# Optimization experiments

Hardware: AMD Instinct MI355X
Metric: run time of the kernel (lower is better)

The kernel has to match this reference:

```python
import jax, jax.numpy as jnp
import numpy as np

V, NJ, NCOMP, NBETA = 778, 16, 24, 10
F_CLOSED, N_ANCHOR = 1554, 32
B, NOBJ = 8, 16384
# MANO kinematic tree parents (wrist + 5 fingers x 3 joints)
PARENTS = np.array([-1, 0, 1, 2, 0, 4, 5, 0, 7, 8, 0, 10, 11, 0, 13, 14])


def setup_inputs() -> dict:
    key = jax.random.key(0)
    ks = jax.random.split(key, 12)
    hand_pose = jax.random.normal(ks[0], (B, 3 + 3 + NCOMP), jnp.float32) * 0.1
    obj_points = jax.random.normal(ks[1], (B, NOBJ, 3), jnp.float32) * 0.1
    hand_beta = jax.random.normal(ks[2], (B, NBETA), jnp.float32) * 0.5
    v_template = jax.random.normal(ks[3], (V, 3), jnp.float32) * 0.05
    shapedirs = jax.random.normal(ks[4], (V, 3, NBETA), jnp.float32) * 0.01
    posedirs = jax.random.normal(ks[5], (V, 3, (NJ - 1) * 9), jnp.float32) * 0.01
    J_regressor = jax.nn.softmax(jax.random.normal(ks[6], (NJ, V), jnp.float32), axis=-1)
    lbs_weights = jax.nn.softmax(jax.random.normal(ks[7], (V, NJ), jnp.float32) * 2.0, axis=-1)
    pca_comps = jax.random.normal(ks[8], (NCOMP, (NJ - 1) * 3), jnp.float32) * 0.1
    anchor_weights = jax.nn.softmax(jax.random.normal(ks[9], (N_ANCHOR, 3), jnp.float32), axis=-1)
    closed_faces = jax.random.randint(ks[10], (F_CLOSED, 3), 0, V, jnp.int32)
    anchor_face_idx = jax.random.randint(ks[11], (N_ANCHOR, 3), 0, V, jnp.int32)
    return dict(hand_pose=hand_pose, obj_points=obj_points, hand_beta=hand_beta,
                v_template=v_template, shapedirs=shapedirs, posedirs=posedirs,
                J_regressor=J_regressor, lbs_weights=lbs_weights, pca_comps=pca_comps,
                anchor_weights=anchor_weights, closed_faces=closed_faces,
                anchor_face_idx=anchor_face_idx)


def rodrigues(r):
    # r: [..., 3] axis-angle -> [..., 3, 3] rotation matrix
    theta = jnp.sqrt(jnp.sum(r * r, axis=-1, keepdims=True) + 1e-16)
    k = r / theta
    c = jnp.cos(theta)[..., None]
    s = jnp.sin(theta)[..., None]
    kx, ky, kz = k[..., 0], k[..., 1], k[..., 2]
    zero = jnp.zeros_like(kx)
    K = jnp.stack([zero, -kz, ky, kz, zero, -kx, -ky, kx, zero], axis=-1)
    K = K.reshape(r.shape[:-1] + (3, 3))
    I = jnp.eye(3, dtype=r.dtype)
    return c * I + s * K + (1.0 - c) * k[..., :, None] * k[..., None, :]


def mano_verts(hand_pose, hand_beta, v_template, shapedirs, posedirs,
               J_regressor, lbs_weights, pca_comps):
    b = hand_pose.shape[0]
    trans = hand_pose[:, :3]
    root = hand_pose[:, 3:6]
    hand45 = hand_pose[:, 6:] @ pca_comps  # PCA -> 45-dim pose (flat_hand_mean: no mean add)
    full = jnp.concatenate([root, hand45], axis=-1).reshape(b, NJ, 3)
    R = rodrigues(full)  # [B,16,3,3]
    v_shaped = v_template + jnp.einsum('vdk,bk->bvd', shapedirs, hand_beta)
    J = jnp.einsum('jv,bvd->bjd', J_regressor, v_shaped)  # [B,16,3]
    pose_feat = (R[:, 1:] - jnp.eye(3, dtype=R.dtype)).reshape(b, (NJ - 1) * 9)
    v_posed = v_shaped + jnp.einsum('vdp,bp->bvd', posedirs, pose_feat)

    def make44(Rj, tj):  # [B,3,3],[B,3] -> [B,4,4]
        T = jnp.zeros((b, 4, 4), R.dtype)
        return T.at[:, :3, :3].set(Rj).at[:, :3, 3].set(tj).at[:, 3, 3].set(1.0)

    Ts = [make44(R[:, 0], J[:, 0])]
    for j in range(1, NJ):  # fixed small kinematic chain
        p = int(PARENTS[j])
        Ts.append(jnp.einsum('bmn,bnk->bmk', Ts[p], make44(R[:, j], J[:, j] - J[:, p])))
    T = jnp.stack(Ts, axis=1)  # [B,16,4,4] global joint transforms
    corr = jnp.einsum('bjmn,bjn->bjm', T[..., :3, :3], J)
    A = T.at[..., :3, 3].add(-corr)  # relative-to-rest transforms
    Tw = jnp.einsum('vj,bjmn->bvmn', lbs_weights, A)  # per-vertex skinning transform
    verts = jnp.einsum('bvmn,bvn->bvm', Tw[..., :3, :3], v_posed) + Tw[..., :3, 3]
    return verts + trans[:, None, :]


def vertex_normals(verts, faces):  # verts [B,V,3], faces [F,3]
    def one(v):
        p0, p1, p2 = v[faces[:, 0]], v[faces[:, 1]], v[faces[:, 2]]
        fn = jnp.cross(p1 - p0, p2 - p0)
        vn = (jnp.zeros_like(v).at[faces[:, 0]].add(fn)
              .at[faces[:, 1]].add(fn).at[faces[:, 2]].add(fn))
        return vn / (jnp.linalg.norm(vn, axis=-1, keepdims=True) + 1e-8)
    return jax.vmap(one)(verts)


def reference(hand_pose, obj_points, hand_beta, v_template, shapedirs, posedirs,
              J_regressor, lbs_weights, pca_comps, anchor_weights,
              closed_faces, anchor_face_idx):
    verts = mano_verts(hand_pose, hand_beta, v_template, shapedirs, posedirs,
                       J_regressor, lbs_weights, pca_comps)  # [B,778,3]
    # get_NN: squared cdist obj->hand + argmin (the memory-bound bottleneck)
    d2 = (jnp.sum(obj_points * obj_points, -1, keepdims=True)
          + jnp.sum(verts * verts, -1)[:, None, :]
          - 2.0 * jnp.einsum('bnd,bvd->bnv', obj_points, verts))  # [B,NOBJ,778]
    nn_idx = jnp.argmin(d2, axis=-1)  # [B,NOBJ]
    nn_dist = jnp.take_along_axis(d2, nn_idx[..., None], axis=-1)[..., 0]
    # contact_map_of_m_to_n
    cmap = 1.0 - 2.0 * (jax.nn.sigmoid(100.0 * nn_dist) - 0.5)
    # inter_penetr_loss: interior obj points (behind nearest hand vertex normal)
    normals = vertex_normals(verts, closed_faces)
    nn_vert = jnp.take_along_axis(verts, nn_idx[..., None], axis=1)
    nn_norm = jnp.take_along_axis(normals, nn_idx[..., None], axis=1)
    interior = jnp.sum((nn_vert - obj_points) * nn_norm, axis=-1) > 0.0
    penetration = jnp.sum(jnp.where(interior, nn_dist, 0.0)) / hand_pose.shape[0]
    # AnchorLayer: barycentric anchor points on the hand surface
    contact_candidates = jnp.einsum('ak,bakd->bad', anchor_weights, verts[:, anchor_face_idx])
    return cmap, penetration, verts, contact_candidates
```

## Files before the change

kernel.cpp:

```cpp
#include <hip/hip_runtime.h>
#include <math.h>

#define NV 778
#define NJ 16
#define NCOMP 24
#define NBETA 10
#define FC 1554
#define NA 32
#define NB 8
#define NOBJ 16384
#define VD (NV*3)
#define BCH 584
#define NVQ 832
#define NG 104
#define NCB 132

__global__ __launch_bounds__(256) void k_blend(
    const float* __restrict__ hp, const float* __restrict__ pca,
    const float* __restrict__ vt, const float* __restrict__ sd,
    const float* __restrict__ pd, const float* __restrict__ beta,
    const float* __restrict__ Jreg,
    float* __restrict__ VP, float* __restrict__ C0, float* __restrict__ C1,
    float* __restrict__ pen)
{
    int bid = blockIdx.x;
    int t = threadIdx.x;
    int wid = t >> 6, lane = t & 63;

    if (bid >= NB*BCH) {
        int o = (bid - NB*BCH)*4 + wid;
        if (o < 528) {
            int jd, k;
            if (o < 48) { jd = o; k = -1; }
            else        { jd = (o-48)/NBETA; k = (o-48)%NBETA; }
            int j = jd/3, d = jd%3;
            const float* jr = Jreg + j*NV;
            float acc = 0.0f;
            for (int v = lane; v < NV; v += 64) {
                float x = (k < 0) ? vt[v*3+d] : sd[(v*3+d)*NBETA + k];
                acc += jr[v] * x;
            }
            #pragma unroll
            for (int off = 32; off; off >>= 1) acc += __shfl_down(acc, off, 64);
            if (lane == 0) { if (k < 0) C0[jd] = acc; else C1[jd*NBETA + k] = acc; }
        }
        return;
    }

    int b = bid / BCH, c = bid % BCH;
    __shared__ float h45[45];
    __shared__ float sR[NJ*9];
    __shared__ float spf[135];

    if (t < 45) {
        float acc = 0.0f;
        #pragma unroll
        for (int k = 0; k < NCOMP; ++k) acc += hp[b*30 + 6 + k] * pca[k*45 + t];
        h45[t] = acc;
    }
    __syncthreads();
    if (t < NJ) {
        float rx, ry, rz;
        if (t == 0) { rx = hp[b*30+3]; ry = hp[b*30+4]; rz = hp[b*30+5]; }
        else        { rx = h45[(t-1)*3]; ry = h45[(t-1)*3+1]; rz = h45[(t-1)*3+2]; }
        float th = sqrtf(rx*rx + ry*ry + rz*rz + 1e-16f);
        float kx = rx/th, ky = ry/th, kz = rz/th;
        float cc = cosf(th), s = sinf(th), o = 1.0f - cc;
        float R[9];
        R[0] = cc + o*kx*kx;     R[1] = -s*kz + o*kx*ky;  R[2] =  s*ky + o*kx*kz;
        R[3] =  s*kz + o*ky*kx;  R[4] = cc + o*ky*ky;     R[5] = -s*kx + o*ky*kz;
        R[6] = -s*ky + o*kz*kx;  R[7] =  s*kx + o*kz*ky;  R[8] = cc + o*kz*kz;
        #pragma unroll
        for (int i = 0; i < 9; ++i) sR[t*9+i] = R[i];
    }
    __syncthreads();
    if (t < 135) {
        int mn = t % 9;
        float d = (mn == 0 || mn == 4 || mn == 8) ? 1.0f : 0.0f;
        spf[t] = sR[9 + t] - d;
    }
    if (bid == 0 && t == 0) *pen = 0.0f;
    __syncthreads();

    int r = c*4 + wid;
    if (r < VD) {
        const float* p  = pd + r * 135;
        float accP = p[lane] * spf[lane] + p[lane+64] * spf[lane+64];
        accP += (lane < 7) ? p[lane+128] * spf[lane+128] : 0.0f;

        float accS = (lane < NBETA) ? sd[r*NBETA + lane] * beta[b*NBETA + lane] : 0.0f;

        #pragma unroll
        for (int off = 32; off; off >>= 1) {
            accP += __shfl_down(accP, off, 64);
            accS += __shfl_down(accS, off, 64);
        }
        if (lane == 0) VP[b*VD + r] = vt[r] + accS + accP;
    }
}

#define PROC1(vk, vidx) {                                                        \
    float d0 = fmaf(-ox0, (vk).x, (vk).w);                                       \
    d0 = fmaf(-oy0, (vk).y, d0); d0 = fmaf(-oz0, (vk).z, d0);                    \
    if (d0 < s0) { s0 = d0; j0 = (vidx); }                                       \
    float d1 = fmaf(-ox1, (vk).x, (vk).w);                                       \
    d1 = fmaf(-oy1, (vk).y, d1); d1 = fmaf(-oz1, (vk).z, d1);                    \
    if (d1 < s1) { s1 = d1; j1 = (vidx); } }

#define PROC8(buf, gbase) {                                                      \
    PROC1((buf)[0], (gbase)+0); PROC1((buf)[1], (gbase)+1);                      \
    PROC1((buf)[2], (gbase)+2); PROC1((buf)[3], (gbase)+3);                      \
    PROC1((buf)[4], (gbase)+4); PROC1((buf)[5], (gbase)+5);                      \
    PROC1((buf)[6], (gbase)+6); PROC1((buf)[7], (gbase)+7); }

__global__ __launch_bounds__(256) void k_mega2(
    const float* __restrict__ hp, const float* __restrict__ pca,
    const float* __restrict__ beta,
    const float* __restrict__ C0, const float* __restrict__ C1,
    const float* __restrict__ W, const float* __restrict__ VP,
    const int* __restrict__ faces, const float* __restrict__ aw,
    const int* __restrict__ afi, const float* __restrict__ obj,
    float* __restrict__ verts, float* __restrict__ cmap,
    float* __restrict__ contact, float* __restrict__ pen)
{
    int blk = blockIdx.x;
    int b = blk >> 5;
    int g = blk & 31;
    int t = threadIdx.x, lane = t & 63, wid = t >> 6;

    __shared__ float4 sPK[NVQ];
    __shared__ float sv[VD];
    __shared__ float sn[VD];
    __shared__ float sR[NJ*9];
    __shared__ float sJ[NJ*3];
    __shared__ float4 sA4[NJ*3];
    __shared__ float h45[45];
    __shared__ float wsum[4];

    int n0 = g*512 + t;
    int n1 = n0 + 256;
    const float* o0p = obj + (b*NOBJ + n0)*3;
    const float* o1p = obj + (b*NOBJ + n1)*3;
    float ox0 = o0p[0], oy0 = o0p[1], oz0 = o0p[2];
    float ox1 = o1p[0], oy1 = o1p[1], oz1 = o1p[2];

    if (t < 45) {
        float acc = 0.0f;
        #pragma unroll
        for (int k = 0; k < NCOMP; ++k) acc += hp[b*30 + 6 + k] * pca[k*45 + t];
        h45[t] = acc;
    }
    for (int i = t; i < VD; i += 256) sn[i] = 0.0f;
    if (t < NVQ - NV) sPK[NV + t] = make_float4(0.f, 0.f, 0.f, 1e30f);
    __syncthreads();

    if (t < NJ) {
        float rx, ry, rz;
        if (t == 0) { rx = hp[b*30+3]; ry = hp[b*30+4]; rz = hp[b*30+5]; }
        else        { rx = h45[(t-1)*3]; ry = h45[(t-1)*3+1]; rz = h45[(t-1)*3+2]; }
        float th = sqrtf(rx*rx + ry*ry + rz*rz + 1e-16f);
        float kx = rx/th, ky = ry/th, kz = rz/th;
        float cc = cosf(th), s = sinf(th), o = 1.0f - cc;
        sR[t*9+0] = cc + o*kx*kx;     sR[t*9+1] = -s*kz + o*kx*ky;  sR[t*9+2] =  s*ky + o*kx*kz;
        sR[t*9+3] =  s*kz + o*ky*kx;  sR[t*9+4] = cc + o*ky*ky;     sR[t*9+5] = -s*kx + o*ky*kz;
        sR[t*9+6] = -s*ky + o*kz*kx;  sR[t*9+7] =  s*kx + o*kz*ky;  sR[t*9+8] = cc + o*kz*kz;
    }
    if (t >= 64 && t < 64 + NJ*3) {
        int o = t - 64;
        float acc = C0[o];
        #pragma unroll
        for (int k = 0; k < NBETA; ++k) acc += C1[o*NBETA + k] * beta[b*NBETA + k];
        sJ[o] = acc;
    }
    __syncthreads();

    if (t < 3) {
        const int par[NJ] = {-1,0,1,2,0,4,5,0,7,8,0,10,11,0,13,14};
        int m = t;
        float Tr[NJ][3], Tt[NJ];
        Tr[0][0] = sR[m*3+0]; Tr[0][1] = sR[m*3+1]; Tr[0][2] = sR[m*3+2];
        Tt[0] = sJ[m];
        #pragma unroll
        for (int j = 1; j < NJ; ++j) {
            int p = par[j];
            float t0 = sJ[j*3+0] - sJ[p*3+0];
            float t1 = sJ[j*3+1] - sJ[p*3+1];
            float t2 = sJ[j*3+2] - sJ[p*3+2];
            float a0 = Tr[p][0], a1 = Tr[p][1], a2 = Tr[p][2];
            #pragma unroll
            for (int n = 0; n < 3; ++n)
                Tr[j][n] = a0*sR[j*9+n] + a1*sR[j*9+3+n] + a2*sR[j*9+6+n];
            Tt[j] = a0*t0 + a1*t1 + a2*t2 + Tt[p];
        }
        #pragma unroll
        for (int j = 0; j < NJ; ++j) {
            float corr = Tr[j][0]*sJ[j*3] + Tr[j][1]*sJ[j*3+1] + Tr[j][2]*sJ[j*3+2];
            sA4[j*3 + m] = make_float4(Tr[j][0], Tr[j][1], Tr[j][2], Tt[j] - corr);
        }
    }
    __syncthreads();

    float tx = hp[b*30+0], ty = hp[b*30+1], tz = hp[b*30+2];
    for (int v = t; v < NV; v += 256) {
        float4 r0 = make_float4(0,0,0,0), r1 = make_float4(0,0,0,0), r2 = make_float4(0,0,0,0);
        const float4* w4 = (const float4*)(W + v * NJ);
        #pragma unroll
        for (int q = 0; q < 4; ++q) {
            float4 wv = w4[q];
            #pragma unroll
            for (int jj = 0; jj < 4; ++jj) {
                int j = q*4 + jj;
                float wj = (jj==0)?wv.x:(jj==1)?wv.y:(jj==2)?wv.z:wv.w;
                float4 A0 = sA4[j*3+0], A1 = sA4[j*3+1], A2 = sA4[j*3+2];
                r0.x += wj*A0.x; r0.y += wj*A0.y; r0.z += wj*A0.z; r0.w += wj*A0.w;
                r1.x += wj*A1.x; r1.y += wj*A1.y; r1.z += wj*A1.z; r1.w += wj*A1.w;
                r2.x += wj*A2.x; r2.y += wj*A2.y; r2.z += wj*A2.z; r2.w += wj*A2.w;
            }
        }
        float px = VP[b*VD + v*3], py = VP[b*VD + v*3+1], pz = VP[b*VD + v*3+2];
        float x = r0.x*px + r0.y*py + r0.z*pz + r0.w + tx;
        float y = r1.x*px + r1.y*py + r1.z*pz + r1.w + ty;
        float z = r2.x*px + r2.y*py + r2.z*pz + r2.w + tz;
        sv[v*3] = x; sv[v*3+1] = y; sv[v*3+2] = z;
        sPK[v] = make_float4(x, y, z, 0.5f*(x*x + y*y + z*z));
        if (g == 0) {
            int i = b*NV + v;
            verts[i*3] = x; verts[i*3+1] = y; verts[i*3+2] = z;
        }
    }
    __syncthreads();

    for (int f = t; f < FC; f += 256) {
        int i0 = faces[f*3], i1 = faces[f*3+1], i2 = faces[f*3+2];
        float ax = sv[i1*3+0]-sv[i0*3+0], ay = sv[i1*3+1]-sv[i0*3+1], az = sv[i1*3+2]-sv[i0*3+2];
        float bx = sv[i2*3+0]-sv[i0*3+0], by = sv[i2*3+1]-sv[i0*3+1], bz = sv[i2*3+2]-sv[i0*3+2];
        float cx = ay*bz - az*by, cy = az*bx - ax*bz, cz = ax*by - ay*bx;
        atomicAdd(&sn[i0*3+0], cx); atomicAdd(&sn[i0*3+1], cy); atomicAdd(&sn[i0*3+2], cz);
        atomicAdd(&sn[i1*3+0], cx); atomicAdd(&sn[i1*3+1], cy); atomicAdd(&sn[i1*3+2], cz);
        atomicAdd(&sn[i2*3+0], cx); atomicAdd(&sn[i2*3+1], cy); atomicAdd(&sn[i2*3+2], cz);
    }
    __syncthreads();

    if (g == 0 && t < NA*3) {
        int a = t / 3, d = t % 3;
        float acc = 0.0f;
        #pragma unroll
        for (int k = 0; k < 3; ++k)
            acc += aw[a*3 + k] * sv[afi[a*3 + k]*3 + d];
        contact[b*NA*3 + t] = acc;
    }

    float s0 = 1e30f, s1 = 1e30f;
    int j0 = 0, j1 = 0;
    {
        float4 A[8], B[8];
        #pragma unroll
        for (int k = 0; k < 8; ++k) A[k] = sPK[k];
        for (int gg = 0; gg + 2 <= NG; gg += 2) {
            #pragma unroll
            for (int k = 0; k < 8; ++k) B[k] = sPK[(gg+1)*8 + k];
            PROC8(A, gg*8);
            if (gg + 2 < NG) {
                #pragma unroll
                for (int k = 0; k < 8; ++k) A[k] = sPK[(gg+2)*8 + k];
            }
            PROC8(B, (gg+1)*8);
        }
    }

    float osq0 = ox0*ox0 + oy0*oy0 + oz0*oz0;
    float d20 = 2.0f * s0 + osq0;
    cmap[b*NOBJ + n0] = 2.0f / (1.0f + __expf(100.0f * d20));
    float4 q0 = sPK[j0];
    float dp0 = (q0.x - ox0)*sn[j0*3+0] + (q0.y - oy0)*sn[j0*3+1] + (q0.z - oz0)*sn[j0*3+2];
    float p = (dp0 > 0.0f) ? d20 : 0.0f;

    float osq1 = ox1*ox1 + oy1*oy1 + oz1*oz1;
    float d21 = 2.0f * s1 + osq1;
    cmap[b*NOBJ + n1] = 2.0f / (1.0f + __expf(100.0f * d21));
    float4 q1 = sPK[j1];
    float dp1 = (q1.x - ox1)*sn[j1*3+0] + (q1.y - oy1)*sn[j1*3+1] + (q1.z - oz1)*sn[j1*3+2];
    p += (dp1 > 0.0f) ? d21 : 0.0f;

    for (int off = 32; off; off >>= 1) p += __shfl_down(p, off, 64);
    if (lane == 0) wsum[wid] = p;
    __syncthreads();
    if (t == 0) atomicAdd(pen, (wsum[0] + wsum[1] + wsum[2] + wsum[3]) * (1.0f / NB));
}

extern "C" void kernel_launch(void* const* d_in, const int* in_sizes, int n_in,
                              void* d_out, int out_size, void* d_ws, size_t ws_size,
                              hipStream_t stream)
{
    const float* hp    = (const float*)d_in[0];
    const float* obj   = (const float*)d_in[1];
    const float* beta  = (const float*)d_in[2];
    const float* vt    = (const float*)d_in[3];
    const float* sd    = (const float*)d_in[4];
    const float* pd    = (const float*)d_in[5];
    const float* Jreg  = (const float*)d_in[6];
    const float* W     = (const float*)d_in[7];
    const float* pca   = (const float*)d_in[8];
    const float* aw    = (const float*)d_in[9];
    const int*   faces = (const int*)d_in[10];
    const int*   afi   = (const int*)d_in[11];

    float* out     = (float*)d_out;
    float* cmap    = out;
    float* pen     = out + NB*NOBJ;
    float* verts   = out + NB*NOBJ + 1;
    float* contact = out + NB*NOBJ + 1 + NB*NV*3;

    float* ws   = (float*)d_ws;
    float* VP   = ws;
    float* C0   = VP + NB*VD;
    float* C1   = C0 + 48;

    k_blend<<<NB*BCH + NCB, 256, 0, stream>>>(hp, pca, vt, sd, pd, beta, Jreg,
                                              VP, C0, C1, pen);
    k_mega2<<<NB*32, 256, 0, stream>>>(hp, pca, beta, C0, C1, W, VP, faces, aw,
                                       afi, obj, verts, cmap, contact, pen);
}
```

Measured before the change: 141.7 us.

## Split mega kernel into skinning, face-normal, and NN kernels to remove redundant work

Before this change, each of the 32 blocks per batch recomputed skinning, vertex positions and face normals for all 778 vertices. The work is now split into three kernels. The first does skinning with each block handling one slice of vertices and writing packed vertices to the workspace. The second accumulates face normals into global memory with atomics and computes the anchor points. The third loads the packed vertices and normals into shared memory and runs the nearest-neighbour search. This removes the 32x redundant per-block preamble, at the cost of two extra launches and a round trip through global memory and global atomics.

```diff
diff --git a/kernel.cpp b/kernel.cpp
--- a/kernel.cpp
+++ b/kernel.cpp
@@ -14,6 +14,9 @@
 #define NVQ 832
 #define NG 104
 #define NCB 132
+#define VSL 25
+#define FSL 49
+#define ZSL 73
 
 __global__ __launch_bounds__(256) void k_blend(
     const float* __restrict__ hp, const float* __restrict__ pca,
@@ -99,59 +102,33 @@
     }
 }
 
-#define PROC1(vk, vidx) {                                                        \
-    float d0 = fmaf(-ox0, (vk).x, (vk).w);                                       \
-    d0 = fmaf(-oy0, (vk).y, d0); d0 = fmaf(-oz0, (vk).z, d0);                    \
-    if (d0 < s0) { s0 = d0; j0 = (vidx); }                                       \
-    float d1 = fmaf(-ox1, (vk).x, (vk).w);                                       \
-    d1 = fmaf(-oy1, (vk).y, d1); d1 = fmaf(-oz1, (vk).z, d1);                    \
-    if (d1 < s1) { s1 = d1; j1 = (vidx); } }
-
-#define PROC8(buf, gbase) {                                                      \
-    PROC1((buf)[0], (gbase)+0); PROC1((buf)[1], (gbase)+1);                      \
-    PROC1((buf)[2], (gbase)+2); PROC1((buf)[3], (gbase)+3);                      \
-    PROC1((buf)[4], (gbase)+4); PROC1((buf)[5], (gbase)+5);                      \
-    PROC1((buf)[6], (gbase)+6); PROC1((buf)[7], (gbase)+7); }
-
-__global__ __launch_bounds__(256) void k_mega2(
+__global__ __launch_bounds__(256) void k_skelp(
     const float* __restrict__ hp, const float* __restrict__ pca,
     const float* __restrict__ beta,
     const float* __restrict__ C0, const float* __restrict__ C1,
     const float* __restrict__ W, const float* __restrict__ VP,
-    const int* __restrict__ faces, const float* __restrict__ aw,
-    const int* __restrict__ afi, const float* __restrict__ obj,
-    float* __restrict__ verts, float* __restrict__ cmap,
-    float* __restrict__ contact, float* __restrict__ pen)
-{
-    int blk = blockIdx.x;
-    int b = blk >> 5;
-    int g = blk & 31;
-    int t = threadIdx.x, lane = t & 63, wid = t >> 6;
-
-    __shared__ float4 sPK[NVQ];
-    __shared__ float sv[VD];
-    __shared__ float sn[VD];
+    float* __restrict__ verts, float4* __restrict__ PK, float* __restrict__ NRM)
+{
+    int k = blockIdx.x;
+    int b = k >> 5, s = k & 31;
+    int t = threadIdx.x;
+    __shared__ float h45[45];
     __shared__ float sR[NJ*9];
     __shared__ float sJ[NJ*3];
     __shared__ float4 sA4[NJ*3];
-    __shared__ float h45[45];
-    __shared__ float wsum[4];
-
-    int n0 = g*512 + t;
-    int n1 = n0 + 256;
-    const float* o0p = obj + (b*NOBJ + n0)*3;
-    const float* o1p = obj + (b*NOBJ + n1)*3;
-    float ox0 = o0p[0], oy0 = o0p[1], oz0 = o0p[2];
-    float ox1 = o1p[0], oy1 = o1p[1], oz1 = o1p[2];
 
     if (t < 45) {
         float acc = 0.0f;
         #pragma unroll
-        for (int k = 0; k < NCOMP; ++k) acc += hp[b*30 + 6 + k] * pca[k*45 + t];
+        for (int kk = 0; kk < NCOMP; ++kk) acc += hp[b*30 + 6 + kk] * pca[kk*45 + t];
         h45[t] = acc;
     }
-    for (int i = t; i < VD; i += 256) sn[i] = 0.0f;
-    if (t < NVQ - NV) sPK[NV + t] = make_float4(0.f, 0.f, 0.f, 1e30f);
+    {
+        int zi = s*ZSL + (t - 128);
+        if (t >= 128 && t < 128 + ZSL && zi - s*ZSL + s*ZSL < VD && zi < VD) NRM[b*VD + zi] = 0.0f;
+    }
+    if (s == 0 && t >= 192 && t < 192 + (NVQ - NV))
+        PK[b*NVQ + NV + (t - 192)] = make_float4(0.f, 0.f, 0.f, 1e30f);
     __syncthreads();
 
     if (t < NJ) {
@@ -160,16 +137,16 @@
         else        { rx = h45[(t-1)*3]; ry = h45[(t-1)*3+1]; rz = h45[(t-1)*3+2]; }
         float th = sqrtf(rx*rx + ry*ry + rz*rz + 1e-16f);
         float kx = rx/th, ky = ry/th, kz = rz/th;
-        float cc = cosf(th), s = sinf(th), o = 1.0f - cc;
-        sR[t*9+0] = cc + o*kx*kx;     sR[t*9+1] = -s*kz + o*kx*ky;  sR[t*9+2] =  s*ky + o*kx*kz;
-        sR[t*9+3] =  s*kz + o*ky*kx;  sR[t*9+4] = cc + o*ky*ky;     sR[t*9+5] = -s*kx + o*ky*kz;
-        sR[t*9+6] = -s*ky + o*kz*kx;  sR[t*9+7] =  s*kx + o*kz*ky;  sR[t*9+8] = cc + o*kz*kz;
+        float cc = cosf(th), sn_ = sinf(th), o = 1.0f - cc;
+        sR[t*9+0] = cc + o*kx*kx;      sR[t*9+1] = -sn_*kz + o*kx*ky;  sR[t*9+2] =  sn_*ky + o*kx*kz;
+        sR[t*9+3] =  sn_*kz + o*ky*kx; sR[t*9+4] = cc + o*ky*ky;       sR[t*9+5] = -sn_*kx + o*ky*kz;
+        sR[t*9+6] = -sn_*ky + o*kz*kx; sR[t*9+7] =  sn_*kx + o*kz*ky;  sR[t*9+8] = cc + o*kz*kz;
     }
     if (t >= 64 && t < 64 + NJ*3) {
         int o = t - 64;
         float acc = C0[o];
         #pragma unroll
-        for (int k = 0; k < NBETA; ++k) acc += C1[o*NBETA + k] * beta[b*NBETA + k];
+        for (int kk = 0; kk < NBETA; ++kk) acc += C1[o*NBETA + kk] * beta[b*NBETA + kk];
         sJ[o] = acc;
     }
     __syncthreads();
@@ -200,55 +177,112 @@
     }
     __syncthreads();
 
-    float tx = hp[b*30+0], ty = hp[b*30+1], tz = hp[b*30+2];
-    for (int v = t; v < NV; v += 256) {
-        float4 r0 = make_float4(0,0,0,0), r1 = make_float4(0,0,0,0), r2 = make_float4(0,0,0,0);
-        const float4* w4 = (const float4*)(W + v * NJ);
-        #pragma unroll
-        for (int q = 0; q < 4; ++q) {
-            float4 wv = w4[q];
+    if (t < VSL) {
+        int v = s*VSL + t;
+        if (v < NV) {
+            float4 r0 = make_float4(0,0,0,0), r1 = make_float4(0,0,0,0), r2 = make_float4(0,0,0,0);
+            const float4* w4 = (const float4*)(W + v * NJ);
             #pragma unroll
-            for (int jj = 0; jj < 4; ++jj) {
-                int j = q*4 + jj;
-                float wj = (jj==0)?wv.x:(jj==1)?wv.y:(jj==2)?wv.z:wv.w;
-                float4 A0 = sA4[j*3+0], A1 = sA4[j*3+1], A2 = sA4[j*3+2];
-                r0.x += wj*A0.x; r0.y += wj*A0.y; r0.z += wj*A0.z; r0.w += wj*A0.w;
-                r1.x += wj*A1.x; r1.y += wj*A1.y; r1.z += wj*A1.z; r1.w += wj*A1.w;
-                r2.x += wj*A2.x; r2.y += wj*A2.y; r2.z += wj*A2.z; r2.w += wj*A2.w;
+            for (int q = 0; q < 4; ++q) {
+                float4 wv = w4[q];
+                #pragma unroll
+                for (int jj = 0; jj < 4; ++jj) {
+                    int j = q*4 + jj;
+                    float wj = (jj==0)?wv.x:(jj==1)?wv.y:(jj==2)?wv.z:wv.w;
+                    float4 A0 = sA4[j*3+0], A1 = sA4[j*3+1], A2 = sA4[j*3+2];
+                    r0.x += wj*A0.x; r0.y += wj*A0.y; r0.z += wj*A0.z; r0.w += wj*A0.w;
+                    r1.x += wj*A1.x; r1.y += wj*A1.y; r1.z += wj*A1.z; r1.w += wj*A1.w;
+                    r2.x += wj*A2.x; r2.y += wj*A2.y; r2.z += wj*A2.z; r2.w += wj*A2.w;
+                }
             }
-        }
-        float px = VP[b*VD + v*3], py = VP[b*VD + v*3+1], pz = VP[b*VD + v*3+2];
-        float x = r0.x*px + r0.y*py + r0.z*pz + r0.w + tx;
-        float y = r1.x*px + r1.y*py + r1.z*pz + r1.w + ty;
-        float z = r2.x*px + r2.y*py + r2.z*pz + r2.w + tz;
-        sv[v*3] = x; sv[v*3+1] = y; sv[v*3+2] = z;
-        sPK[v] = make_float4(x, y, z, 0.5f*(x*x + y*y + z*z));
-        if (g == 0) {
+            float tx = hp[b*30+0], ty = hp[b*30+1], tz = hp[b*30+2];
+            float px = VP[b*VD + v*3], py = VP[b*VD + v*3+1], pz = VP[b*VD + v*3+2];
+            float x = r0.x*px + r0.y*py + r0.z*pz + r0.w + tx;
+            float y = r1.x*px + r1.y*py + r1.z*pz + r1.w + ty;
+            float z = r2.x*px + r2.y*py + r2.z*pz + r2.w + tz;
             int i = b*NV + v;
             verts[i*3] = x; verts[i*3+1] = y; verts[i*3+2] = z;
-        }
-    }
-    __syncthreads();
-
-    for (int f = t; f < FC; f += 256) {
-        int i0 = faces[f*3], i1 = faces[f*3+1], i2 = faces[f*3+2];
-        float ax = sv[i1*3+0]-sv[i0*3+0], ay = sv[i1*3+1]-sv[i0*3+1], az = sv[i1*3+2]-sv[i0*3+2];
-        float bx = sv[i2*3+0]-sv[i0*3+0], by = sv[i2*3+1]-sv[i0*3+1], bz = sv[i2*3+2]-sv[i0*3+2];
-        float cx = ay*bz - az*by, cy = az*bx - ax*bz, cz = ax*by - ay*bx;
-        atomicAdd(&sn[i0*3+0], cx); atomicAdd(&sn[i0*3+1], cy); atomicAdd(&sn[i0*3+2], cz);
-        atomicAdd(&sn[i1*3+0], cx); atomicAdd(&sn[i1*3+1], cy); atomicAdd(&sn[i1*3+2], cz);
-        atomicAdd(&sn[i2*3+0], cx); atomicAdd(&sn[i2*3+1], cy); atomicAdd(&sn[i2*3+2], cz);
-    }
-    __syncthreads();
-
-    if (g == 0 && t < NA*3) {
-        int a = t / 3, d = t % 3;
+            PK[b*NVQ + v] = make_float4(x, y, z, 0.5f*(x*x + y*y + z*z));
+        }
+    }
+}
+
+__global__ __launch_bounds__(256) void k_faces(
+    const int* __restrict__ faces, const float4* __restrict__ PK,
+    const float* __restrict__ aw, const int* __restrict__ afi,
+    float* __restrict__ NRM, float* __restrict__ contact)
+{
+    int k = blockIdx.x;
+    int b = k >> 5, s = k & 31;
+    int t = threadIdx.x;
+
+    if (t < FSL) {
+        int f = s*FSL + t;
+        if (f < FC) {
+            int i0 = faces[f*3], i1 = faces[f*3+1], i2 = faces[f*3+2];
+            float4 p0 = PK[b*NVQ + i0];
+            float4 p1 = PK[b*NVQ + i1];
+            float4 p2 = PK[b*NVQ + i2];
+            float ax = p1.x-p0.x, ay = p1.y-p0.y, az = p1.z-p0.z;
+            float bx = p2.x-p0.x, by = p2.y-p0.y, bz = p2.z-p0.z;
+            float cx = ay*bz - az*by, cy = az*bx - ax*bz, cz = ax*by - ay*bx;
+            float* nb = NRM + b*VD;
+            atomicAdd(nb + i0*3+0, cx); atomicAdd(nb + i0*3+1, cy); atomicAdd(nb + i0*3+2, cz);
+            atomicAdd(nb + i1*3+0, cx); atomicAdd(nb + i1*3+1, cy); atomicAdd(nb + i1*3+2, cz);
+            atomicAdd(nb + i2*3+0, cx); atomicAdd(nb + i2*3+1, cy); atomicAdd(nb + i2*3+2, cz);
+        }
+    }
+    if (s == 0 && t >= 64 && t < 64 + NA*3) {
+        int a = (t-64) / 3, d = (t-64) % 3;
         float acc = 0.0f;
         #pragma unroll
-        for (int k = 0; k < 3; ++k)
-            acc += aw[a*3 + k] * sv[afi[a*3 + k]*3 + d];
-        contact[b*NA*3 + t] = acc;
-    }
+        for (int kk = 0; kk < 3; ++kk) {
+            const float* pv = (const float*)(PK + b*NVQ + afi[a*3 + kk]);
+            acc += aw[a*3 + kk] * pv[d];
+        }
+        contact[b*NA*3 + t - 64] = acc;
+    }
+}
+
+#define PROC1(vk, vidx) {                                                        \
+    float d0 = fmaf(-ox0, (vk).x, (vk).w);                                       \
+    d0 = fmaf(-oy0, (vk).y, d0); d0 = fmaf(-oz0, (vk).z, d0);                    \
+    if (d0 < s0) { s0 = d0; j0 = (vidx); }                                       \
+    float d1 = fmaf(-ox1, (vk).x, (vk).w);                                       \
+    d1 = fmaf(-oy1, (vk).y, d1); d1 = fmaf(-oz1, (vk).z, d1);                    \
+    if (d1 < s1) { s1 = d1; j1 = (vidx); } }
+
+#define PROC8(buf, gbase) {                                                      \
+    PROC1((buf)[0], (gbase)+0); PROC1((buf)[1], (gbase)+1);                      \
+    PROC1((buf)[2], (gbase)+2); PROC1((buf)[3], (gbase)+3);                      \
+    PROC1((buf)[4], (gbase)+4); PROC1((buf)[5], (gbase)+5);                      \
+    PROC1((buf)[6], (gbase)+6); PROC1((buf)[7], (gbase)+7); }
+
+__global__ __launch_bounds__(256) void k_nn(const float* __restrict__ obj,
+                                            const float4* __restrict__ PK,
+                                            const float* __restrict__ NRM,
+                                            float* __restrict__ cmap,
+                                            float* __restrict__ pen)
+{
+    int blk = blockIdx.x;
+    int b = blk >> 5;
+    int g = blk & 31;
+    int t = threadIdx.x, lane = t & 63, wid = t >> 6;
+
+    __shared__ float4 sPK[NVQ];
+    __shared__ float sNRM[VD];
+    __shared__ float wsum[4];
+
+    int n0 = g*512 + t;
+    int n1 = n0 + 256;
+    const float* o0p = obj + (b*NOBJ + n0)*3;
+    const float* o1p = obj + (b*NOBJ + n1)*3;
+    float ox0 = o0p[0], oy0 = o0p[1], oz0 = o0p[2];
+    float ox1 = o1p[0], oy1 = o1p[1], oz1 = o1p[2];
+
+    for (int i = t; i < NVQ; i += 256) sPK[i] = PK[b*NVQ + i];
+    for (int i = t; i < VD; i += 256) sNRM[i] = NRM[b*VD + i];
+    __syncthreads();
 
     float s0 = 1e30f, s1 = 1e30f;
     int j0 = 0, j1 = 0;
@@ -272,14 +306,16 @@
     float d20 = 2.0f * s0 + osq0;
     cmap[b*NOBJ + n0] = 2.0f / (1.0f + __expf(100.0f * d20));
     float4 q0 = sPK[j0];
-    float dp0 = (q0.x - ox0)*sn[j0*3+0] + (q0.y - oy0)*sn[j0*3+1] + (q0.z - oz0)*sn[j0*3+2];
+    float dp0 = (q0.x - ox0)*sNRM[j0*3+0] + (q0.y - oy0)*sNRM[j0*3+1]
+              + (q0.z - oz0)*sNRM[j0*3+2];
     float p = (dp0 > 0.0f) ? d20 : 0.0f;
 
     float osq1 = ox1*ox1 + oy1*oy1 + oz1*oz1;
     float d21 = 2.0f * s1 + osq1;
     cmap[b*NOBJ + n1] = 2.0f / (1.0f + __expf(100.0f * d21));
     float4 q1 = sPK[j1];
-    float dp1 = (q1.x - ox1)*sn[j1*3+0] + (q1.y - oy1)*sn[j1*3+1] + (q1.z - oz1)*sn[j1*3+2];
+    float dp1 = (q1.x - ox1)*sNRM[j1*3+0] + (q1.y - oy1)*sNRM[j1*3+1]
+              + (q1.z - oz1)*sNRM[j1*3+2];
     p += (dp1 > 0.0f) ? d21 : 0.0f;
 
     for (int off = 32; off; off >>= 1) p += __shfl_down(p, off, 64);
@@ -312,12 +348,16 @@
     float* contact = out + NB*NOBJ + 1 + NB*NV*3;
 
     float* ws   = (float*)d_ws;
-    float* VP   = ws;
+    float4* PK  = (float4*)ws;
+    float* NRM  = ws + NB*NVQ*4;
+    float* VP   = NRM + NB*VD;
     float* C0   = VP + NB*VD;
     float* C1   = C0 + 48;
 
     k_blend<<<NB*BCH + NCB, 256, 0, stream>>>(hp, pca, vt, sd, pd, beta, Jreg,
                                               VP, C0, C1, pen);
-    k_mega2<<<NB*32, 256, 0, stream>>>(hp, pca, beta, C0, C1, W, VP, faces, aw,
-                                       afi, obj, verts, cmap, contact, pen);
-}
+    k_skelp<<<NB*32, 256, 0, stream>>>(hp, pca, beta, C0, C1, W, VP,
+                                       verts, PK, NRM);
+    k_faces<<<NB*32, 256, 0, stream>>>(faces, PK, aw, afi, NRM, contact);
+    k_nn   <<<NB*32, 256, 0, stream>>>(obj, PK, NRM, cmap, pen);
+}
```

New measurement: 133.7 us. 5.6% less time.

## Split skinning into separate kernel and dual-source NN search from LDS and global

Applied to the files above, without the earlier changes.

The fused kernel is split in two. A new skinning kernel spreads the 778 vertices across 32 blocks per batch instead of every block redundantly skinning all vertices, and writes packed vertex data to a workspace. The NN kernel then loads the packed vertices into LDS and computes normals and anchors from them. It scans the first half of the vertices from LDS and the second half directly from global memory (L1/L2) with two independent argmin chains, aiming to balance LDS and cache bandwidth. This adds a kernel launch and a global round-trip, and merging the two chains on ties keeps the lower (LDS-half) index, which matches the original ordering.

```diff
diff --git a/kernel.cpp b/kernel.cpp
--- a/kernel.cpp
+++ b/kernel.cpp
@@ -12,8 +12,10 @@
 #define VD (NV*3)
 #define BCH 584
 #define NVQ 832
-#define NG 104
+#define HALF 416
+#define HG 52
 #define NCB 132
+#define VSL 25
 
 __global__ __launch_bounds__(256) void k_blend(
     const float* __restrict__ hp, const float* __restrict__ pca,
@@ -99,59 +101,29 @@
     }
 }
 
-#define PROC1(vk, vidx) {                                                        \
-    float d0 = fmaf(-ox0, (vk).x, (vk).w);                                       \
-    d0 = fmaf(-oy0, (vk).y, d0); d0 = fmaf(-oz0, (vk).z, d0);                    \
-    if (d0 < s0) { s0 = d0; j0 = (vidx); }                                       \
-    float d1 = fmaf(-ox1, (vk).x, (vk).w);                                       \
-    d1 = fmaf(-oy1, (vk).y, d1); d1 = fmaf(-oz1, (vk).z, d1);                    \
-    if (d1 < s1) { s1 = d1; j1 = (vidx); } }
-
-#define PROC8(buf, gbase) {                                                      \
-    PROC1((buf)[0], (gbase)+0); PROC1((buf)[1], (gbase)+1);                      \
-    PROC1((buf)[2], (gbase)+2); PROC1((buf)[3], (gbase)+3);                      \
-    PROC1((buf)[4], (gbase)+4); PROC1((buf)[5], (gbase)+5);                      \
-    PROC1((buf)[6], (gbase)+6); PROC1((buf)[7], (gbase)+7); }
-
-__global__ __launch_bounds__(256) void k_mega2(
+__global__ __launch_bounds__(256) void k_skelp(
     const float* __restrict__ hp, const float* __restrict__ pca,
     const float* __restrict__ beta,
     const float* __restrict__ C0, const float* __restrict__ C1,
     const float* __restrict__ W, const float* __restrict__ VP,
-    const int* __restrict__ faces, const float* __restrict__ aw,
-    const int* __restrict__ afi, const float* __restrict__ obj,
-    float* __restrict__ verts, float* __restrict__ cmap,
-    float* __restrict__ contact, float* __restrict__ pen)
+    float* __restrict__ verts, float4* __restrict__ PK)
 {
-    int blk = blockIdx.x;
-    int b = blk >> 5;
-    int g = blk & 31;
-    int t = threadIdx.x, lane = t & 63, wid = t >> 6;
-
-    __shared__ float4 sPK[NVQ];
-    __shared__ float sv[VD];
-    __shared__ float sn[VD];
+    int k = blockIdx.x;
+    int b = k >> 5, s = k & 31;
+    int t = threadIdx.x;
+    __shared__ float h45[45];
     __shared__ float sR[NJ*9];
     __shared__ float sJ[NJ*3];
     __shared__ float4 sA4[NJ*3];
-    __shared__ float h45[45];
-    __shared__ float wsum[4];
-
-    int n0 = g*512 + t;
-    int n1 = n0 + 256;
-    const float* o0p = obj + (b*NOBJ + n0)*3;
-    const float* o1p = obj + (b*NOBJ + n1)*3;
-    float ox0 = o0p[0], oy0 = o0p[1], oz0 = o0p[2];
-    float ox1 = o1p[0], oy1 = o1p[1], oz1 = o1p[2];
 
     if (t < 45) {
         float acc = 0.0f;
         #pragma unroll
-        for (int k = 0; k < NCOMP; ++k) acc += hp[b*30 + 6 + k] * pca[k*45 + t];
+        for (int kk = 0; kk < NCOMP; ++kk) acc += hp[b*30 + 6 + kk] * pca[kk*45 + t];
         h45[t] = acc;
     }
-    for (int i = t; i < VD; i += 256) sn[i] = 0.0f;
-    if (t < NVQ - NV) sPK[NV + t] = make_float4(0.f, 0.f, 0.f, 1e30f);
+    if (s == 0 && t >= 192 && t < 192 + (NVQ - NV))
+        PK[b*NVQ + NV + (t - 192)] = make_float4(0.f, 0.f, 0.f, 1e30f);
     __syncthreads();
 
     if (t < NJ) {
@@ -160,16 +132,16 @@
         else        { rx = h45[(t-1)*3]; ry = h45[(t-1)*3+1]; rz = h45[(t-1)*3+2]; }
         float th = sqrtf(rx*rx + ry*ry + rz*rz + 1e-16f);
         float kx = rx/th, ky = ry/th, kz = rz/th;
-        float cc = cosf(th), s = sinf(th), o = 1.0f - cc;
-        sR[t*9+0] = cc + o*kx*kx;     sR[t*9+1] = -s*kz + o*kx*ky;  sR[t*9+2] =  s*ky + o*kx*kz;
-        sR[t*9+3] =  s*kz + o*ky*kx;  sR[t*9+4] = cc + o*ky*ky;     sR[t*9+5] = -s*kx + o*ky*kz;
-        sR[t*9+6] = -s*ky + o*kz*kx;  sR[t*9+7] =  s*kx + o*kz*ky;  sR[t*9+8] = cc + o*kz*kz;
+        float cc = cosf(th), sn_ = sinf(th), o = 1.0f - cc;
+        sR[t*9+0] = cc + o*kx*kx;      sR[t*9+1] = -sn_*kz + o*kx*ky;  sR[t*9+2] =  sn_*ky + o*kx*kz;
+        sR[t*9+3] =  sn_*kz + o*ky*kx; sR[t*9+4] = cc + o*ky*ky;       sR[t*9+5] = -sn_*kx + o*ky*kz;
+        sR[t*9+6] = -sn_*ky + o*kz*kx; sR[t*9+7] =  sn_*kx + o*kz*ky;  sR[t*9+8] = cc + o*kz*kz;
     }
     if (t >= 64 && t < 64 + NJ*3) {
         int o = t - 64;
         float acc = C0[o];
         #pragma unroll
-        for (int k = 0; k < NBETA; ++k) acc += C1[o*NBETA + k] * beta[b*NBETA + k];
+        for (int kk = 0; kk < NBETA; ++kk) acc += C1[o*NBETA + kk] * beta[b*NBETA + kk];
         sJ[o] = acc;
     }
     __syncthreads();
@@ -200,73 +172,129 @@
     }
     __syncthreads();
 
-    float tx = hp[b*30+0], ty = hp[b*30+1], tz = hp[b*30+2];
-    for (int v = t; v < NV; v += 256) {
-        float4 r0 = make_float4(0,0,0,0), r1 = make_float4(0,0,0,0), r2 = make_float4(0,0,0,0);
-        const float4* w4 = (const float4*)(W + v * NJ);
-        #pragma unroll
-        for (int q = 0; q < 4; ++q) {
-            float4 wv = w4[q];
+    if (t < VSL) {
+        int v = s*VSL + t;
+        if (v < NV) {
+            float4 r0 = make_float4(0,0,0,0), r1 = make_float4(0,0,0,0), r2 = make_float4(0,0,0,0);
+            const float4* w4 = (const float4*)(W + v * NJ);
             #pragma unroll
-            for (int jj = 0; jj < 4; ++jj) {
-                int j = q*4 + jj;
-                float wj = (jj==0)?wv.x:(jj==1)?wv.y:(jj==2)?wv.z:wv.w;
-                float4 A0 = sA4[j*3+0], A1 = sA4[j*3+1], A2 = sA4[j*3+2];
-                r0.x += wj*A0.x; r0.y += wj*A0.y; r0.z += wj*A0.z; r0.w += wj*A0.w;
-                r1.x += wj*A1.x; r1.y += wj*A1.y; r1.z += wj*A1.z; r1.w += wj*A1.w;
-                r2.x += wj*A2.x; r2.y += wj*A2.y; r2.z += wj*A2.z; r2.w += wj*A2.w;
+            for (int q = 0; q < 4; ++q) {
+                float4 wv = w4[q];
+                #pragma unroll
+                for (int jj = 0; jj < 4; ++jj) {
+                    int j = q*4 + jj;
+                    float wj = (jj==0)?wv.x:(jj==1)?wv.y:(jj==2)?wv.z:wv.w;
+                    float4 A0 = sA4[j*3+0], A1 = sA4[j*3+1], A2 = sA4[j*3+2];
+                    r0.x += wj*A0.x; r0.y += wj*A0.y; r0.z += wj*A0.z; r0.w += wj*A0.w;
+                    r1.x += wj*A1.x; r1.y += wj*A1.y; r1.z += wj*A1.z; r1.w += wj*A1.w;
+                    r2.x += wj*A2.x; r2.y += wj*A2.y; r2.z += wj*A2.z; r2.w += wj*A2.w;
+                }
             }
-        }
-        float px = VP[b*VD + v*3], py = VP[b*VD + v*3+1], pz = VP[b*VD + v*3+2];
-        float x = r0.x*px + r0.y*py + r0.z*pz + r0.w + tx;
-        float y = r1.x*px + r1.y*py + r1.z*pz + r1.w + ty;
-        float z = r2.x*px + r2.y*py + r2.z*pz + r2.w + tz;
-        sv[v*3] = x; sv[v*3+1] = y; sv[v*3+2] = z;
-        sPK[v] = make_float4(x, y, z, 0.5f*(x*x + y*y + z*z));
-        if (g == 0) {
+            float tx = hp[b*30+0], ty = hp[b*30+1], tz = hp[b*30+2];
+            float px = VP[b*VD + v*3], py = VP[b*VD + v*3+1], pz = VP[b*VD + v*3+2];
+            float x = r0.x*px + r0.y*py + r0.z*pz + r0.w + tx;
+            float y = r1.x*px + r1.y*py + r1.z*pz + r1.w + ty;
+            float z = r2.x*px + r2.y*py + r2.z*pz + r2.w + tz;
             int i = b*NV + v;
             verts[i*3] = x; verts[i*3+1] = y; verts[i*3+2] = z;
-        }
-    }
+            PK[b*NVQ + v] = make_float4(x, y, z, 0.5f*(x*x + y*y + z*z));
+        }
+    }
+}
+
+#define PROC1X(vk, vidx, ss0, jj0, ss1, jj1) {                                   \
+    float d0 = fmaf(-ox0, (vk).x, (vk).w);                                       \
+    d0 = fmaf(-oy0, (vk).y, d0); d0 = fmaf(-oz0, (vk).z, d0);                    \
+    if (d0 < ss0) { ss0 = d0; jj0 = (vidx); }                                    \
+    float d1 = fmaf(-ox1, (vk).x, (vk).w);                                       \
+    d1 = fmaf(-oy1, (vk).y, d1); d1 = fmaf(-oz1, (vk).z, d1);                    \
+    if (d1 < ss1) { ss1 = d1; jj1 = (vidx); } }
+
+#define PROC8X(buf, gbase, ss0, jj0, ss1, jj1) {                                 \
+    PROC1X((buf)[0], (gbase)+0, ss0, jj0, ss1, jj1);                             \
+    PROC1X((buf)[1], (gbase)+1, ss0, jj0, ss1, jj1);                             \
+    PROC1X((buf)[2], (gbase)+2, ss0, jj0, ss1, jj1);                             \
+    PROC1X((buf)[3], (gbase)+3, ss0, jj0, ss1, jj1);                             \
+    PROC1X((buf)[4], (gbase)+4, ss0, jj0, ss1, jj1);                             \
+    PROC1X((buf)[5], (gbase)+5, ss0, jj0, ss1, jj1);                             \
+    PROC1X((buf)[6], (gbase)+6, ss0, jj0, ss1, jj1);                             \
+    PROC1X((buf)[7], (gbase)+7, ss0, jj0, ss1, jj1); }
+
+__global__ __launch_bounds__(256) void k_nn(const float* __restrict__ obj,
+                                            const float4* __restrict__ PK,
+                                            const int* __restrict__ faces,
+                                            const float* __restrict__ aw,
+                                            const int* __restrict__ afi,
+                                            float* __restrict__ cmap,
+                                            float* __restrict__ contact,
+                                            float* __restrict__ pen)
+{
+    int blk = blockIdx.x;
+    int b = blk >> 5;
+    int g = blk & 31;
+    int t = threadIdx.x, lane = t & 63, wid = t >> 6;
+
+    __shared__ float4 sPK[NVQ];
+    __shared__ float sn[VD];
+    __shared__ float wsum[4];
+
+    int n0 = g*512 + t;
+    int n1 = n0 + 256;
+    const float* o0p = obj + (b*NOBJ + n0)*3;
+    const float* o1p = obj + (b*NOBJ + n1)*3;
+    float ox0 = o0p[0], oy0 = o0p[1], oz0 = o0p[2];
+    float ox1 = o1p[0], oy1 = o1p[1], oz1 = o1p[2];
+
+    for (int i = t; i < NVQ; i += 256) sPK[i] = PK[b*NVQ + i];
+    for (int i = t; i < VD; i += 256) sn[i] = 0.0f;
     __syncthreads();
 
     for (int f = t; f < FC; f += 256) {
         int i0 = faces[f*3], i1 = faces[f*3+1], i2 = faces[f*3+2];
-        float ax = sv[i1*3+0]-sv[i0*3+0], ay = sv[i1*3+1]-sv[i0*3+1], az = sv[i1*3+2]-sv[i0*3+2];
-        float bx = sv[i2*3+0]-sv[i0*3+0], by = sv[i2*3+1]-sv[i0*3+1], bz = sv[i2*3+2]-sv[i0*3+2];
+        float4 p0 = sPK[i0], p1 = sPK[i1], p2 = sPK[i2];
+        float ax = p1.x-p0.x, ay = p1.y-p0.y, az = p1.z-p0.z;
+        float bx = p2.x-p0.x, by = p2.y-p0.y, bz = p2.z-p0.z;
         float cx = ay*bz - az*by, cy = az*bx - ax*bz, cz = ax*by - ay*bx;
         atomicAdd(&sn[i0*3+0], cx); atomicAdd(&sn[i0*3+1], cy); atomicAdd(&sn[i0*3+2], cz);
         atomicAdd(&sn[i1*3+0], cx); atomicAdd(&sn[i1*3+1], cy); atomicAdd(&sn[i1*3+2], cz);
         atomicAdd(&sn[i2*3+0], cx); atomicAdd(&sn[i2*3+1], cy); atomicAdd(&sn[i2*3+2], cz);
     }
-    __syncthreads();
-
     if (g == 0 && t < NA*3) {
         int a = t / 3, d = t % 3;
         float acc = 0.0f;
         #pragma unroll
-        for (int k = 0; k < 3; ++k)
-            acc += aw[a*3 + k] * sv[afi[a*3 + k]*3 + d];
+        for (int kk = 0; kk < 3; ++kk) {
+            float4 pv = sPK[afi[a*3 + kk]];
+            acc += aw[a*3 + kk] * ((d==0)?pv.x:(d==1)?pv.y:pv.z);
+        }
         contact[b*NA*3 + t] = acc;
     }
-
-    float s0 = 1e30f, s1 = 1e30f;
-    int j0 = 0, j1 = 0;
+    __syncthreads();
+
+    const float4* __restrict__ gp = PK + b*NVQ + HALF;
+    float sL0 = 1e30f, sL1 = 1e30f, sG0 = 1e30f, sG1 = 1e30f;
+    int   jL0 = 0,     jL1 = 0,     jG0 = HALF,  jG1 = HALF;
     {
-        float4 A[8], B[8];
-        #pragma unroll
-        for (int k = 0; k < 8; ++k) A[k] = sPK[k];
-        for (int gg = 0; gg + 2 <= NG; gg += 2) {
+        float4 LA[8], LB[8], GA[8], GB[8];
+        #pragma unroll
+        for (int k = 0; k < 8; ++k) { LA[k] = sPK[k]; GA[k] = gp[k]; }
+        for (int gg = 0; gg + 2 <= HG; gg += 2) {
             #pragma unroll
-            for (int k = 0; k < 8; ++k) B[k] = sPK[(gg+1)*8 + k];
-            PROC8(A, gg*8);
-            if (gg + 2 < NG) {
+            for (int k = 0; k < 8; ++k) { LB[k] = sPK[(gg+1)*8 + k]; GB[k] = gp[(gg+1)*8 + k]; }
+            PROC8X(LA, gg*8,        sL0, jL0, sL1, jL1);
+            PROC8X(GA, HALF+gg*8,   sG0, jG0, sG1, jG1);
+            if (gg + 2 < HG) {
                 #pragma unroll
-                for (int k = 0; k < 8; ++k) A[k] = sPK[(gg+2)*8 + k];
+                for (int k = 0; k < 8; ++k) { LA[k] = sPK[(gg+2)*8 + k]; GA[k] = gp[(gg+2)*8 + k]; }
             }
-            PROC8(B, (gg+1)*8);
-        }
-    }
+            PROC8X(LB, (gg+1)*8,      sL0, jL0, sL1, jL1);
+            PROC8X(GB, HALF+(gg+1)*8, sG0, jG0, sG1, jG1);
+        }
+    }
+    float s0 = sL0; int j0 = jL0;
+    if (sG0 < s0) { s0 = sG0; j0 = jG0; }
+    float s1 = sL1; int j1 = jL1;
+    if (sG1 < s1) { s1 = sG1; j1 = jG1; }
 
     float osq0 = ox0*ox0 + oy0*oy0 + oz0*oz0;
     float d20 = 2.0f * s0 + osq0;
@@ -312,12 +340,14 @@
     float* contact = out + NB*NOBJ + 1 + NB*NV*3;
 
     float* ws   = (float*)d_ws;
-    float* VP   = ws;
+    float4* PK  = (float4*)ws;
+    float* VP   = ws + NB*NVQ*4;
     float* C0   = VP + NB*VD;
     float* C1   = C0 + 48;
 
     k_blend<<<NB*BCH + NCB, 256, 0, stream>>>(hp, pca, vt, sd, pd, beta, Jreg,
                                               VP, C0, C1, pen);
-    k_mega2<<<NB*32, 256, 0, stream>>>(hp, pca, beta, C0, C1, W, VP, faces, aw,
-                                       afi, obj, verts, cmap, contact, pen);
+    k_skelp<<<NB*32, 256, 0, stream>>>(hp, pca, beta, C0, C1, W, VP, verts, PK);
+    k_nn   <<<NB*32, 256, 0, stream>>>(obj, PK, faces, aw, afi,
+                                       cmap, contact, pen);
 }
```

After: 148.8 us. 1.05x slower.
